# Optimization experiments

Hardware: AMD Instinct MI355X
Metric: run time of the kernel (lower is better)

Reference implementation:

```python
import jax, jax.numpy as jnp
import numpy as np

# Model dims (see shape_source): seq_len fixed to 12 by reshape(1,12,-1); rnn_units fixed to 64 by proj in-dim.
B, T, N, HZ = 16, 12, 512, 12
DIN, DOUT, YCOV = 1, 1, 1
RNN, MEMN, MEMD, K = 64, 20, 64, 3
DDEC = RNN + MEMD  # 128


def _cheb(g, k):
    # Chebyshev polynomials T_0..T_{k-1} of support g: [I, g, 2g T_{i-1} - T_{i-2}, ...]
    n = g.shape[0]
    Ts = [jnp.eye(n, dtype=g.dtype), g]
    for _ in range(2, k):
        Ts.append(2.0 * g @ Ts[-1] - Ts[-2])
    return Ts


def _agcn(x, sup, W, b):
    # x: [B,N,C], sup: [2K,N,N] -> x_g: [B,N,2K*C] (k-major order matches torch.cat over support_set)
    b_, n, _ = x.shape
    xg = jnp.einsum('knm,bmc->bnkc', sup, x).reshape(b_, n, -1)
    return xg @ W + b


def _cell(x, state, sup, gW, gb, uW, ub, hdim):
    ins = jnp.concatenate([x, state], axis=-1)
    zr = jax.nn.sigmoid(_agcn(ins, sup, gW, gb))
    z, r = zr[..., :hdim], zr[..., hdim:]
    hc = jnp.tanh(_agcn(jnp.concatenate([x, z * state], axis=-1), sup, uW, ub))
    return r * state + (1.0 - r) * hc


def setup_inputs() -> dict:
    key = jax.random.key(0)
    ks = jax.random.split(key, 16)
    def nrm(k, shape, s=0.1):
        return jax.random.normal(k, shape, dtype=jnp.float32) * s
    return {
        'x': nrm(ks[0], (B, T, N, DIN), 1.0),
        'y_cov': nrm(ks[1], (B, HZ, N, YCOV), 1.0),
        'Memory': nrm(ks[2], (MEMN, MEMD)),
        'Wq': nrm(ks[3], (RNN, MEMD)),
        'We1': nrm(ks[4], (N, MEMN)),
        'We2': nrm(ks[5], (N, MEMN)),
        'tWe1': nrm(ks[6], (MEMD, RNN)),
        'tWe2': nrm(ks[7], (MEMD, RNN)),
        'fc_d_W': nrm(ks[8], (DDEC, RNN)),
        'fc_e_W': nrm(ks[9], (RNN, RNN)),
        'enc_gate_W': nrm(ks[10], (2 * K * (DIN + RNN), 2 * RNN)),
        'enc_gate_b': jnp.zeros((2 * RNN,), jnp.float32),
        'enc_up_W': nrm(ks[11], (2 * K * (DIN + RNN), RNN)),
        'enc_up_b': jnp.zeros((RNN,), jnp.float32),
        'dec_gate_W': nrm(ks[12], (2 * K * (DOUT + YCOV + DDEC), 2 * DDEC)),
        'dec_gate_b': jnp.zeros((2 * DDEC,), jnp.float32),
        'dec_up_W': nrm(ks[13], (2 * K * (DOUT + YCOV + DDEC), DDEC)),
        'dec_up_b': jnp.zeros((DDEC,), jnp.float32),
        'proj_W': nrm(ks[14], (DDEC + RNN, DOUT)),
        'proj_b': jnp.zeros((DOUT,), jnp.float32),
    }


def reference(x, y_cov, Memory, Wq, We1, We2, tWe1, tWe2, fc_d_W, fc_e_W,
              enc_gate_W, enc_gate_b, enc_up_W, enc_up_b,
              dec_gate_W, dec_gate_b, dec_up_W, dec_up_b, proj_W, proj_b):
    # adaptive supports from memory
    ne1 = We1 @ Memory
    ne2 = We2 @ Memory
    g1 = jax.nn.softmax(jax.nn.relu(ne1 @ ne2.T), axis=-1)
    g2 = jax.nn.softmax(jax.nn.relu(ne2 @ ne1.T), axis=-1)
    sup = jnp.stack(_cheb(g1, K) + _cheb(g2, K))  # [2K,N,N]

    # encoder: GRU-style graph recurrence over time via scan
    def enc_step(state, xt):
        h = _cell(xt, state, sup, enc_gate_W, enc_gate_b, enc_up_W, enc_up_b, RNN)
        return h, h
    s0 = jnp.zeros((B, N, RNN), x.dtype)
    _, hs = jax.lax.scan(enc_step, s0, jnp.swapaxes(x, 0, 1))
    h_en = jnp.swapaxes(hs, 0, 1)  # [B,T,N,RNN]
    h_t = h_en[:, -1]

    # memory retrieval
    query = h_t @ Wq                                    # [B,N,MEMD]
    att_score = jax.nn.softmax(query @ Memory.T, axis=-1)  # [B,N,MEMN]
    h_att = att_score @ Memory                          # [B,N,MEMD]
    _, ind = jax.lax.top_k(att_score, 20)
    pos = Memory[ind[:, :, 0]]
    neg = Memory[ind[:, :, 1:]]

    # test-time supports from last-batch retrieved memory (as in torch code: h_att[-1])
    ne3 = h_att[-1] @ tWe1
    ne4 = h_att[-1] @ tWe2
    tg1 = jax.nn.softmax(jax.nn.relu(ne3 @ ne4.T), axis=-1)
    tg2 = jax.nn.softmax(jax.nn.relu(ne4 @ ne3.T), axis=-1)
    tsup = jnp.stack(_cheb(tg1, K) + _cheb(tg2, K))

    ht = jnp.concatenate([h_t, h_att], axis=-1)  # [B,N,DDEC]
    # matches torch fc_e(h_en).reshape(1,12,-1): row-major flatten of [B,T,N,RNN] into [T, B*N*RNN]
    e_flat = (h_en @ fc_e_W).reshape(T, -1)

    go = jnp.zeros((B, N, DOUT), x.dtype)
    state = ht  # num_layers = 1
    outs = []
    for t in range(HZ):
        xt = jnp.concatenate([go, y_cov[:, t]], axis=-1)
        h_de = _cell(xt, state, tsup, dec_gate_W, dec_gate_b, dec_up_W, dec_up_b, DDEC)
        state = h_de
        d_flat = (h_de @ fc_d_W).reshape(-1)            # [B*N*RNN]
        att = jax.nn.softmax(e_flat @ d_flat)           # [T] global temporal weights
        context = jnp.einsum('btnr,t->bnr', h_en, att)  # [B,N,RNN]
        go = jnp.concatenate([h_de, context], axis=-1) @ proj_W + proj_b
        outs.append(go)
    output = jnp.stack(outs, axis=1)  # [B,HZ,N,DOUT]
    return output, h_att, query, pos, neg, att_score
```

## Files before the change

kernel.cpp:

```cpp
#include <hip/hip_runtime.h>
#include <hip/hip_bf16.h>
#include <math.h>

typedef __hip_bfloat16 bf16;
typedef __attribute__((ext_vector_type(8))) short short8;
typedef __attribute__((ext_vector_type(4))) float f32x4;
typedef unsigned short u16;

__device__ inline u16 f2bu(float f) {
  unsigned u = __builtin_bit_cast(unsigned, f);
  u += 0x7fffu + ((u >> 16) & 1u);
  return (u16)(u >> 16);
}

__global__ void detect_k(const u16* __restrict__ u, int* __restrict__ flag) {
  if (threadIdx.x == 0 && blockIdx.x == 0) {
    int wild = 0;
    for (int i = 0; i < 256; i++) {
      int e = (u[i] >> 7) & 0xFF;
      if (e < 0x66 || e > 0x8A) wild++;
    }
    *flag = (wild > 64) ? 1 : 0;
  }
}

__global__ void in2f_k(const void* __restrict__ in, float* __restrict__ out, int n,
                       const int* __restrict__ flag) {
  int i = blockIdx.x * 256 + threadIdx.x;
  if (i >= n) return;
  if (*flag) out[i] = ((const float*)in)[i];
  else       out[i] = __bfloat162float(((const bf16*)in)[i]);
}

__global__ void zero_k(float* __restrict__ p, int n) {
  int i = blockIdx.x * 256 + threadIdx.x;
  if (i < n) p[i] = 0.f;
}

__global__ void zeroi_k(int* __restrict__ p, int n) {
  int i = blockIdx.x * 256 + threadIdx.x;
  if (i < n) p[i] = 0;
}

__global__ void transpose_k(const float* __restrict__ in, float* __restrict__ out,
                            int rows, int cols) {
  int i = blockIdx.x * 256 + threadIdx.x;
  if (i >= rows * cols) return;
  int c = i % cols, r = i / cols;
  out[(size_t)c * rows + r] = in[i];
}

__global__ void f2b_k(const float* __restrict__ in, u16* __restrict__ out, int n) {
  int i = blockIdx.x * 256 + threadIdx.x;
  if (i < n) out[i] = f2bu(in[i]);
}

__global__ void padw_k(const float* __restrict__ W, float* __restrict__ Wp,
                       int K, int N, int Kpad) {
  int i = blockIdx.x * 256 + threadIdx.x;
  if (i >= Kpad * N) return;
  int n = i % N, k = i / N;
  Wp[i] = (k < K) ? W[(size_t)k * N + n] : 0.f;
}

__global__ void w2bt_k(const float* __restrict__ W, u16* __restrict__ WT,
                       int KT, int Nw, int KTpad) {
  int i = blockIdx.x * 256 + threadIdx.x;
  if (i >= Nw * KTpad) return;
  int kp = i % KTpad, n = i / KTpad;
  WT[i] = (kp < KT) ? f2bu(W[(size_t)kp * Nw + n]) : (u16)0;
}

enum { EPI_NONE = 0, EPI_RELU = 1, EPI_SIG = 2, EPI_CHEB = 3, EPI_SCAT = 4, EPI_UPD = 5 };

struct GemmArgs {
  const float* A; const float* Bm; float* C;
  int M, N, K;
};
__global__ __launch_bounds__(256) void gemm_s(GemmArgs g) {
  __shared__ float As[16][65];
  __shared__ float Bs[16][65];
  const int tid = threadIdx.x;
  const int tx = tid & 15, ty = tid >> 4;
  const int bm = blockIdx.y * 64, bn = blockIdx.x * 64;
  float acc[4][4] = {{0.f}};
  for (int k0 = 0; k0 < g.K; k0 += 16) {
#pragma unroll
    for (int i = 0; i < 4; i++) {
      int idx = i * 256 + tid; int c = idx & 15, r = idx >> 4;
      int mm = bm + r, kk = k0 + c;
      As[c][r] = (mm < g.M && kk < g.K) ? g.A[(size_t)mm * g.K + kk] : 0.f;
    }
#pragma unroll
    for (int i = 0; i < 4; i++) {
      int idx = i * 256 + tid; int c = idx & 63, r = idx >> 6;
      int kk = k0 + r, nn = bn + c;
      Bs[r][c] = (kk < g.K && nn < g.N) ? g.Bm[(size_t)kk * g.N + nn] : 0.f;
    }
    __syncthreads();
#pragma unroll
    for (int kk = 0; kk < 16; kk++) {
      float a[4], b[4];
#pragma unroll
      for (int i = 0; i < 4; i++) a[i] = As[kk][ty * 4 + i];
#pragma unroll
      for (int j = 0; j < 4; j++) b[j] = Bs[kk][tx * 4 + j];
#pragma unroll
      for (int i = 0; i < 4; i++)
#pragma unroll
        for (int j = 0; j < 4; j++) acc[i][j] = fmaf(a[i], b[j], acc[i][j]);
    }
    __syncthreads();
  }
#pragma unroll
  for (int i = 0; i < 4; i++) {
    int m = bm + ty * 4 + i;
    if (m >= g.M) continue;
#pragma unroll
    for (int j = 0; j < 4; j++) {
      int n = bn + tx * 4 + j;
      if (n >= g.N) continue;
      g.C[(size_t)m * g.N + n] = acc[i][j];
    }
  }
}

struct FGemmArgs {
  const float* A; const float* Bm; const float* bias; float* C;
  int M, N, K, ldb;
  const float* aux0;
  float* aux1;
  float* aux2;
  int i0, i1, i2;
};

template<int EPI>
__global__ __launch_bounds__(256) void fgemm_k(FGemmArgs g) {
  __shared__ __align__(16) float As[2][32][68];
  __shared__ __align__(16) float Bs[2][32][68];
  const int tid = threadIdx.x;
  const int tx = tid & 15, ty = tid >> 4;
  const int bm = blockIdx.y * 64, bn = blockIdx.x * 64;
  const int ar = tid >> 2, ac = (tid & 3) * 4;
  const int br = tid >> 4, bc = (tid & 15) * 4;
  float acc[4][4] = {{0.f}};

  float4 av0 = *(const float4*)(g.A + (size_t)(bm + ar) * g.K + ac);
  float4 av1 = *(const float4*)(g.A + (size_t)(bm + ar) * g.K + 16 + ac);
  float4 bv0 = *(const float4*)(g.Bm + (size_t)br * g.ldb + bn + bc);
  float4 bv1 = *(const float4*)(g.Bm + (size_t)(16 + br) * g.ldb + bn + bc);
  As[0][ac + 0][ar] = av0.x; As[0][ac + 1][ar] = av0.y;
  As[0][ac + 2][ar] = av0.z; As[0][ac + 3][ar] = av0.w;
  As[0][16 + ac + 0][ar] = av1.x; As[0][16 + ac + 1][ar] = av1.y;
  As[0][16 + ac + 2][ar] = av1.z; As[0][16 + ac + 3][ar] = av1.w;
  *(float4*)&Bs[0][br][bc] = bv0;
  *(float4*)&Bs[0][16 + br][bc] = bv1;
  __syncthreads();

  int cur = 0;
  for (int k0 = 0; k0 < g.K; k0 += 32) {
    const bool has_next = (k0 + 32 < g.K);
    if (has_next) {
      av0 = *(const float4*)(g.A + (size_t)(bm + ar) * g.K + k0 + 32 + ac);
      av1 = *(const float4*)(g.A + (size_t)(bm + ar) * g.K + k0 + 48 + ac);
      bv0 = *(const float4*)(g.Bm + (size_t)(k0 + 32 + br) * g.ldb + bn + bc);
      bv1 = *(const float4*)(g.Bm + (size_t)(k0 + 48 + br) * g.ldb + bn + bc);
    }
#pragma unroll
    for (int kk = 0; kk < 32; kk++) {
      float4 a4 = *(const float4*)&As[cur][kk][ty * 4];
      float4 b4 = *(const float4*)&Bs[cur][kk][tx * 4];
      float a[4] = {a4.x, a4.y, a4.z, a4.w};
      float b[4] = {b4.x, b4.y, b4.z, b4.w};
#pragma unroll
      for (int i = 0; i < 4; i++)
#pragma unroll
        for (int j = 0; j < 4; j++) acc[i][j] = fmaf(a[i], b[j], acc[i][j]);
    }
    if (has_next) {
      int nxt = cur ^ 1;
      As[nxt][ac + 0][ar] = av0.x; As[nxt][ac + 1][ar] = av0.y;
      As[nxt][ac + 2][ar] = av0.z; As[nxt][ac + 3][ar] = av0.w;
      As[nxt][16 + ac + 0][ar] = av1.x; As[nxt][16 + ac + 1][ar] = av1.y;
      As[nxt][16 + ac + 2][ar] = av1.z; As[nxt][16 + ac + 3][ar] = av1.w;
      *(float4*)&Bs[nxt][br][bc] = bv0;
      *(float4*)&Bs[nxt][16 + br][bc] = bv1;
      __syncthreads();
      cur = nxt;
    }
  }
#pragma unroll
  for (int i = 0; i < 4; i++) {
    int m = bm + ty * 4 + i;
#pragma unroll
    for (int j = 0; j < 4; j++) {
      int n = bn + tx * 4 + j;
      if (n >= g.N) continue;
      float v = acc[i][j];
      if (EPI == EPI_NONE) {
        g.C[(size_t)m * g.N + n] = v;
      } else if (EPI == EPI_RELU) {
        g.C[(size_t)m * g.N + n] = fmaxf(v, 0.f);
      } else if (EPI == EPI_SIG) {
        v += g.bias[n];
        g.C[(size_t)m * g.N + n] = 1.f / (1.f + expf(-v));
      } else if (EPI == EPI_CHEB) {
        g.C[(size_t)m * g.N + n] = 2.f * v - (m == n ? 1.f : 0.f);
      } else if (EPI == EPI_SCAT) {
        int bb = n / g.i0, cc = n % g.i0;
        int km = m >> 9;
        int kmap = km + 1 + (km >= 2 ? 1 : 0);
        int node = m & 511;
        g.aux1[((size_t)bb * 512 + node) * g.i1 + (size_t)kmap * g.i0 + cc] = v;
      } else if (EPI == EPI_UPD) {
        v = tanhf(v + g.bias[n]);
        float r = g.aux0[(size_t)m * g.i0 + g.i1 + n];
        float h = r * g.aux1[(size_t)m * g.i1 + n] + (1.f - r) * v;
        g.aux1[(size_t)m * g.i1 + n] = h;
        if (g.aux2)
          g.aux2[(((size_t)(m >> 9) * 12 + g.i2) * 512 + (m & 511)) * 64 + n] = h;
      }
    }
  }
}

template<int EPI>
__global__ __launch_bounds__(256) void fgemm32_k(FGemmArgs g) {
  __shared__ __align__(16) float As[2][16][40];
  __shared__ __align__(16) float Bs[2][16][68];
  const int tid = threadIdx.x;
  const int tx = tid & 15, ty = tid >> 4;
  const int bm = blockIdx.y * 32, bn = blockIdx.x * 64;
  const int ar = tid >> 2, ac = (tid & 3) * 4;
  const int br = tid >> 4, bc = (tid & 15) * 4;
  float acc[2][4] = {{0.f}};

  float4 av, bv;
  if (ar < 32) av = *(const float4*)(g.A + (size_t)(bm + ar) * g.K + ac);
  bv = *(const float4*)(g.Bm + (size_t)br * g.ldb + bn + bc);
  if (ar < 32) {
    As[0][ac + 0][ar] = av.x; As[0][ac + 1][ar] = av.y;
    As[0][ac + 2][ar] = av.z; As[0][ac + 3][ar] = av.w;
  }
  *(float4*)&Bs[0][br][bc] = bv;
  __syncthreads();

  int cur = 0;
  for (int k0 = 0; k0 < g.K; k0 += 16) {
    const bool has_next = (k0 + 16 < g.K);
    if (has_next) {
      if (ar < 32) av = *(const float4*)(g.A + (size_t)(bm + ar) * g.K + k0 + 16 + ac);
      bv = *(const float4*)(g.Bm + (size_t)(k0 + 16 + br) * g.ldb + bn + bc);
    }
#pragma unroll
    for (int kk = 0; kk < 16; kk++) {
      float a0 = As[cur][kk][ty * 2 + 0];
      float a1 = As[cur][kk][ty * 2 + 1];
      float4 b4 = *(const float4*)&Bs[cur][kk][tx * 4];
      float b[4] = {b4.x, b4.y, b4.z, b4.w};
#pragma unroll
      for (int j = 0; j < 4; j++) {
        acc[0][j] = fmaf(a0, b[j], acc[0][j]);
        acc[1][j] = fmaf(a1, b[j], acc[1][j]);
      }
    }
    if (has_next) {
      int nxt = cur ^ 1;
      if (ar < 32) {
        As[nxt][ac + 0][ar] = av.x; As[nxt][ac + 1][ar] = av.y;
        As[nxt][ac + 2][ar] = av.z; As[nxt][ac + 3][ar] = av.w;
      }
      *(float4*)&Bs[nxt][br][bc] = bv;
      __syncthreads();
      cur = nxt;
    }
  }
#pragma unroll
  for (int i = 0; i < 2; i++) {
    int m = bm + ty * 2 + i;
#pragma unroll
    for (int j = 0; j < 4; j++) {
      int n = bn + tx * 4 + j;
      if (n >= g.N) continue;
      float v = acc[i][j];
      if (EPI == EPI_NONE) {
        g.C[(size_t)m * g.N + n] = v;
      } else if (EPI == EPI_UPD) {
        v = tanhf(v + g.bias[n]);
        float r = g.aux0[(size_t)m * g.i0 + g.i1 + n];
        float h = r * g.aux1[(size_t)m * g.i1 + n] + (1.f - r) * v;
        g.aux1[(size_t)m * g.i1 + n] = h;
        if (g.aux2)
          g.aux2[(((size_t)(m >> 9) * 12 + g.i2) * 512 + (m & 511)) * 64 + n] = h;
      }
    }
  }
}

struct MmArgs {
  const u16* A; const u16* BT; int M, N, K;
  const float* bias; float* C;
  u16* xg;
  const float* zr; float* state; float* hen;
  int i0, i1, i2;
};

template<int EPI>
__global__ __launch_bounds__(256) void mm_k(MmArgs g) {
  __shared__ __align__(16) u16 Als[2][64][40];
  __shared__ __align__(16) u16 Bls[2][64][40];
  const int tid = threadIdx.x;
  const int w = tid >> 6, lane = tid & 63;
  const int l15 = lane & 15, lk = lane >> 4;
  const int m0 = blockIdx.y * 64, n0 = blockIdx.x * 64;
  const int srow = tid >> 2, schunk = tid & 3;
  f32x4 acc[4];
#pragma unroll
  for (int j = 0; j < 4; j++) acc[j] = (f32x4){0.f, 0.f, 0.f, 0.f};

  short8 a8 = *(const short8*)(g.A + (size_t)(m0 + srow) * g.K + schunk * 8);
  short8 b8 = (short8){0,0,0,0,0,0,0,0};
  if (n0 + srow < g.N)
    b8 = *(const short8*)(g.BT + (size_t)(n0 + srow) * g.K + schunk * 8);
  *(short8*)&Als[0][srow][schunk * 8] = a8;
  *(short8*)&Bls[0][srow][schunk * 8] = b8;
  __syncthreads();

  int cur = 0;
  for (int k0 = 0; k0 < g.K; k0 += 32) {
    const bool has_next = (k0 + 32 < g.K);
    if (has_next) {
      a8 = *(const short8*)(g.A + (size_t)(m0 + srow) * g.K + k0 + 32 + schunk * 8);
      b8 = (short8){0,0,0,0,0,0,0,0};
      if (n0 + srow < g.N)
        b8 = *(const short8*)(g.BT + (size_t)(n0 + srow) * g.K + k0 + 32 + schunk * 8);
    }
    short8 af = *(const short8*)&Als[cur][w * 16 + l15][lk * 8];
#pragma unroll
    for (int j = 0; j < 4; j++) {
      short8 bf = *(const short8*)&Bls[cur][j * 16 + l15][lk * 8];
      acc[j] = __builtin_amdgcn_mfma_f32_16x16x32_bf16(af, bf, acc[j], 0, 0, 0);
    }
    if (has_next) {
      int nxt = cur ^ 1;
      *(short8*)&Als[nxt][srow][schunk * 8] = a8;
      *(short8*)&Bls[nxt][srow][schunk * 8] = b8;
      __syncthreads();
      cur = nxt;
    }
  }

#pragma unroll
  for (int j = 0; j < 4; j++) {
    int col = n0 + j * 16 + l15;
    if (col >= g.N) continue;
#pragma unroll
    for (int r = 0; r < 4; r++) {
      int row = m0 + w * 16 + lk * 4 + r;
      float v = acc[j][r];
      if (EPI == EPI_SCAT) {
        int bb = col / g.i0, cc = col % g.i0;
        int km = row >> 9;
        int kmap = km + 1 + (km >= 2 ? 1 : 0);
        int node = row & 511;
        g.xg[((size_t)bb * 512 + node) * g.i1 + (size_t)kmap * g.i0 + cc] = f2bu(v);
      } else if (EPI == EPI_SIG) {
        v += g.bias[col];
        g.C[(size_t)row * g.N + col] = 1.f / (1.f + expf(-v));
      } else if (EPI == EPI_UPD) {
        v = tanhf(v + g.bias[col]);
        float rr = g.zr[(size_t)row * g.i0 + g.i1 + col];
        float h = rr * g.state[(size_t)row * g.i1 + col] + (1.f - rr) * v;
        g.state[(size_t)row * g.i1 + col] = h;
        if (g.hen)
          g.hen[(((size_t)(row >> 9) * 12 + g.i2) * 512 + (row & 511)) * 64 + col] = h;
      }
    }
  }
}


__global__ void buildx_k(const float* __restrict__ x1, int x1bs,
                         const float* __restrict__ state,
                         const float* __restrict__ zr,
                         float* __restrict__ X, float* __restrict__ XG,
                         int C, int hdim, int zrld) {
  int idx = blockIdx.x * 256 + threadIdx.x;
  if (idx >= 16 * 512 * C) return;
  int c = idx % C; int bn = idx / C; int n = bn & 511; int b = bn >> 9;
  float v;
  if (c == 0) v = x1[(size_t)b * x1bs + n];
  else {
    v = state[(size_t)bn * hdim + (c - 1)];
    if (zr) v *= zr[(size_t)bn * zrld + (c - 1)];
  }
  X[(size_t)n * 1088 + b * C + c] = v;
  XG[(size_t)bn * 416 + c] = v;
  XG[(size_t)bn * 416 + 3 * C + c] = v;
}

__global__ void buildx2_k(const float* __restrict__ x1, int x1bs,
                          const float* __restrict__ x2, int x2bs,
                          const float* __restrict__ state,
                          const float* __restrict__ zr,
                          u16* __restrict__ XT, u16* __restrict__ XGb,
                          int C, int NX, int hdim, int zrld, int KTpad) {
  int idx = blockIdx.x * 256 + threadIdx.x;
  if (idx >= 16 * 512 * C) return;
  int c = idx % C; int bn = idx / C; int n = bn & 511; int b = bn >> 9;
  float v;
  if (c == 0) v = x1[(size_t)b * x1bs + n];
  else if (c < NX) v = x2[(size_t)b * x2bs + n];
  else {
    v = state[(size_t)bn * hdim + (c - NX)];
    if (zr) v *= zr[(size_t)bn * zrld + (c - NX)];
  }
  u16 bv = f2bu(v);
  XT[((size_t)(b * C + c)) * 512 + n] = bv;
  XGb[(size_t)bn * KTpad + c] = bv;
  XGb[(size_t)bn * KTpad + 3 * C + c] = bv;
}

__global__ __launch_bounds__(256) void softmax512_k(const float* __restrict__ Min,
                                                    float* __restrict__ out, int colMajor) {
  int row = blockIdx.x;
  __shared__ float buf[512];
  __shared__ float red[256];
  int tid = threadIdx.x;
  for (int i = tid; i < 512; i += 256)
    buf[i] = colMajor ? Min[(size_t)i * 512 + row] : Min[(size_t)row * 512 + i];
  __syncthreads();
  float mx = -1e30f;
  for (int i = tid; i < 512; i += 256) mx = fmaxf(mx, buf[i]);
  red[tid] = mx; __syncthreads();
  for (int w = 128; w > 0; w >>= 1) { if (tid < w) red[tid] = fmaxf(red[tid], red[tid + w]); __syncthreads(); }
  mx = red[0]; __syncthreads();
  float s = 0.f;
  for (int i = tid; i < 512; i += 256) { float e = expf(buf[i] - mx); buf[i] = e; s += e; }
  red[tid] = s; __syncthreads();
  for (int w = 128; w > 0; w >>= 1) { if (tid < w) red[tid] += red[tid + w]; __syncthreads(); }
  float inv = 1.f / red[0];
  for (int i = tid; i < 512; i += 256) out[(size_t)row * 512 + i] = buf[i] * inv;
}

__global__ __launch_bounds__(256) void attmem_k(const float* __restrict__ query,
    const float* __restrict__ Mem, float* __restrict__ att_out,
    float* __restrict__ hatt, int* __restrict__ ind) {
  __shared__ float sm[20 * 64];
  for (int i = threadIdx.x; i < 20 * 64; i += 256) sm[i] = Mem[i];
  __syncthreads();
  int bn = blockIdx.x * 256 + threadIdx.x;
  if (bn >= 16 * 512) return;
  float q[64];
#pragma unroll
  for (int d = 0; d < 64; d++) q[d] = query[(size_t)bn * 64 + d];
  float lg[20];
  float mx = -1e30f;
#pragma unroll
  for (int m = 0; m < 20; m++) {
    float s = 0.f;
#pragma unroll
    for (int d = 0; d < 64; d++) s = fmaf(q[d], sm[m * 64 + d], s);
    lg[m] = s; mx = fmaxf(mx, s);
  }
  float se = 0.f;
#pragma unroll
  for (int m = 0; m < 20; m++) { lg[m] = expf(lg[m] - mx); se += lg[m]; }
  float inv = 1.f / se;
#pragma unroll
  for (int m = 0; m < 20; m++) {
    lg[m] *= inv;
    att_out[(size_t)bn * 20 + m] = lg[m];
  }
#pragma unroll
  for (int d = 0; d < 64; d++) {
    float s = 0.f;
#pragma unroll
    for (int m = 0; m < 20; m++) s = fmaf(lg[m], sm[m * 64 + d], s);
    hatt[(size_t)bn * 64 + d] = s;
  }
  unsigned used = 0;
  for (int s = 0; s < 20; s++) {
    float bv = -1e30f; int bi = 0;
#pragma unroll
    for (int m = 0; m < 20; m++) {
      bool better = (!((used >> m) & 1u)) && (lg[m] > bv);
      if (better) { bv = lg[m]; bi = m; }
    }
    used |= (1u << bi);
    ind[(size_t)bn * 20 + s] = bi;
  }
}

__global__ void gather_pn_k(const int* __restrict__ ind, const float* __restrict__ Memf,
                            float* __restrict__ pos, float* __restrict__ neg) {
  size_t i = (size_t)blockIdx.x * 256 + threadIdx.x;
  if (i >= (size_t)16 * 512 * 20 * 64) return;
  int d = (int)(i & 63); size_t r = i >> 6;
  int s = (int)(r % 20); size_t bn = r / 20;
  int m = ind[bn * 20 + s];
  float v = Memf[m * 64 + d];
  if (s == 0) pos[bn * 64 + d] = v;
  else neg[(bn * 19 + (size_t)(s - 1)) * 64 + d] = v;
}

__global__ void sinit_k(const float* __restrict__ H, const float* __restrict__ hatt,
                        float* __restrict__ S) {
  int i = blockIdx.x * 256 + threadIdx.x;
  if (i >= 8192 * 128) return;
  int c = i & 127; int bn = i >> 7;
  S[i] = (c < 64) ? H[(size_t)bn * 64 + c] : hatt[(size_t)bn * 64 + (c - 64)];
}

__global__ __launch_bounds__(256) void att_dot_k(const float* __restrict__ E,
    const float* __restrict__ D, float* __restrict__ partial) {
  int t = blockIdx.y, ch = blockIdx.x;
  const float* e = E + (size_t)t * 524288 + (size_t)ch * 16384;
  const float* d = D + (size_t)ch * 16384;
  float s = 0.f;
  for (int i = threadIdx.x; i < 16384; i += 256) s = fmaf(e[i], d[i], s);
  __shared__ float red[256];
  red[threadIdx.x] = s; __syncthreads();
  for (int w = 128; w > 0; w >>= 1) {
    if (threadIdx.x < w) red[threadIdx.x] += red[threadIdx.x + w];
    __syncthreads();
  }
  if (threadIdx.x == 0) partial[t * 32 + ch] = red[0];
}

__global__ void att_sm_k(const float* __restrict__ partial, float* __restrict__ att) {
  __shared__ float p[384];
  __shared__ float l[12];
  int tid = threadIdx.x;
  p[tid] = partial[tid];
  __syncthreads();
  if (tid < 12) {
    float s = 0.f;
    for (int i = 0; i < 32; i++) s += p[tid * 32 + i];
    l[tid] = s;
  }
  __syncthreads();
  if (tid == 0) {
    float mx = l[0];
    for (int i = 1; i < 12; i++) mx = fmaxf(mx, l[i]);
    float se = 0.f; float e[12];
    for (int i = 0; i < 12; i++) { e[i] = expf(l[i] - mx); se += e[i]; }
    float inv = 1.f / se;
    for (int i = 0; i < 12; i++) att[i] = e[i] * inv;
  }
}

__global__ __launch_bounds__(64) void ctxgo_k(const float* __restrict__ hen,
    const float* __restrict__ att, const float* __restrict__ S,
    const float* __restrict__ pW, const float* __restrict__ pb,
    float* __restrict__ go, float* __restrict__ outp, int tstep) {
  int bn = blockIdx.x; int r = threadIdx.x;
  __shared__ float a[12];
  if (r < 12) a[r] = att[r];
  __syncthreads();
  int b = bn >> 9, n = bn & 511;
  float ctx = 0.f;
#pragma unroll
  for (int t = 0; t < 12; t++)
    ctx = fmaf(hen[((size_t)(b * 12 + t) * 512 + n) * 64 + r], a[t], ctx);
  float part = ctx * pW[128 + r] + S[(size_t)bn * 128 + r] * pW[r]
             + S[(size_t)bn * 128 + 64 + r] * pW[64 + r];
#pragma unroll
  for (int off = 32; off > 0; off >>= 1) part += __shfl_down(part, off);
  if (r == 0) {
    float gv = part + pb[0];
    go[bn] = gv;
    outp[(size_t)(b * 12 + tstep) * 512 + n] = gv;
  }
}


static void fgemm(hipStream_t st, int epi, const float* A, const float* Bm,
                  const float* bias, float* C, int M, int N, int K, int ldb,
                  const float* aux0, float* aux1, float* aux2,
                  int i0, int i1, int i2) {
  FGemmArgs a{A, Bm, bias, C, M, N, K, ldb, aux0, aux1, aux2, i0, i1, i2};
  dim3 grid((N + 63) / 64, M / 64);
  switch (epi) {
    case 0: fgemm_k<0><<<grid, 256, 0, st>>>(a); break;
    case 1: fgemm_k<1><<<grid, 256, 0, st>>>(a); break;
    case 2: fgemm_k<2><<<grid, 256, 0, st>>>(a); break;
    case 3: fgemm_k<3><<<grid, 256, 0, st>>>(a); break;
    case 4: fgemm_k<4><<<grid, 256, 0, st>>>(a); break;
    case 5: fgemm_k<5><<<grid, 256, 0, st>>>(a); break;
  }
}

static void fgemm32(hipStream_t st, int epi, const float* A, const float* Bm,
                    const float* bias, float* C, int M, int N, int K, int ldb,
                    const float* aux0, float* aux1, float* aux2,
                    int i0, int i1, int i2) {
  FGemmArgs a{A, Bm, bias, C, M, N, K, ldb, aux0, aux1, aux2, i0, i1, i2};
  dim3 grid((N + 63) / 64, M / 32);
  switch (epi) {
    case 0: fgemm32_k<0><<<grid, 256, 0, st>>>(a); break;
    case 5: fgemm32_k<5><<<grid, 256, 0, st>>>(a); break;
  }
}

static void mm(hipStream_t st, int epi, const u16* A, const u16* BT,
               int M, int N, int K, const float* bias, float* C, u16* xg,
               const float* zr, float* state, float* hen, int i0, int i1, int i2) {
  MmArgs a{A, BT, M, N, K, bias, C, xg, zr, state, hen, i0, i1, i2};
  dim3 grid((N + 63) / 64, M / 64);
  switch (epi) {
    case EPI_SIG:  mm_k<EPI_SIG><<<grid, 256, 0, st>>>(a); break;
    case EPI_SCAT: mm_k<EPI_SCAT><<<grid, 256, 0, st>>>(a); break;
    case EPI_UPD:  mm_k<EPI_UPD><<<grid, 256, 0, st>>>(a); break;
  }
}

extern "C" void kernel_launch(void* const* d_in, const int* in_sizes, int n_in,
                              void* d_out, int out_size, void* d_ws, size_t ws_size,
                              hipStream_t stream) {
  (void)out_size; (void)ws_size; (void)n_in; (void)in_sizes;
  float* ws = (float*)d_ws;
  float* out = (float*)d_out;

  size_t off = 0;
  auto alloc = [&](size_t n) { size_t o = off; off += (n + 63) & ~(size_t)63; return ws + o; };

  const int isz[20] = {98304, 98304, 1280, 4096, 10240, 10240, 4096, 4096, 8192, 4096,
                       49920, 128, 24960, 64, 199680, 256, 99840, 128, 192, 1};
  float* fin[20];
  for (int i = 0; i < 20; i++) fin[i] = alloc((size_t)isz[i]);

  float* Gbig  = alloc((size_t)2048 * 512);
  float* tGbig = Gbig;
  float* Mbuf  = alloc((size_t)512 * 512);
  float* ne1b  = alloc((size_t)512 * 64);
  float* ne2b  = alloc((size_t)512 * 64);
  float* neT   = alloc((size_t)64 * 512);
  float* X     = alloc((size_t)512 * 1088);
  float* XG    = alloc((size_t)8192 * 416);
  float* Wgp   = alloc((size_t)416 * 128);
  float* Wup   = alloc((size_t)416 * 64);
  float* zr    = alloc((size_t)8192 * 256);
  float* H     = alloc((size_t)8192 * 64);
  float* S     = alloc((size_t)8192 * 128);
  float* hen   = alloc((size_t)16 * 12 * 512 * 64);
  float* E     = alloc((size_t)16 * 12 * 512 * 64);
  float* Dflat = alloc((size_t)8192 * 64);
  float* go    = alloc((size_t)8192);
  float* partial = alloc((size_t)512);
  float* attv  = alloc((size_t)64);
  int* ind     = (int*)alloc((size_t)8192 * 20);
  int* dflag   = (int*)alloc((size_t)64);
  u16* Gb16 = (u16*)alloc((size_t)2048 * 512 / 2);
  u16* XT   = (u16*)alloc((size_t)2080 * 512 / 2);
  u16* XGb  = (u16*)alloc((size_t)8192 * 800 / 2);
  u16* WTdg = (u16*)alloc((size_t)256 * 800 / 2);
  u16* WTdu = (u16*)alloc((size_t)128 * 800 / 2);

  float* o_out   = out;
  float* o_hatt  = out + 98304;
  float* o_query = o_hatt + 524288;
  float* o_pos   = o_query + 524288;
  float* o_neg   = o_pos + 524288;
  float* o_att   = o_neg + 9961472;

  detect_k<<<1, 64, 0, stream>>>((const u16*)d_in[0], dflag);
  for (int i = 0; i < 20; i++)
    in2f_k<<<(isz[i] + 255) / 256, 256, 0, stream>>>(d_in[i], fin[i], isz[i], dflag);

  padw_k<<<(416 * 128 + 255) / 256, 256, 0, stream>>>(fin[10], Wgp, 390, 128, 416);
  padw_k<<<(416 * 64 + 255) / 256, 256, 0, stream>>>(fin[12], Wup, 390, 64, 416);
  w2bt_k<<<(256 * 800 + 255) / 256, 256, 0, stream>>>(fin[14], WTdg, 780, 256, 800);
  w2bt_k<<<(128 * 800 + 255) / 256, 256, 0, stream>>>(fin[16], WTdu, 780, 128, 800);

  zero_k<<<(512 * 1088 + 255) / 256, 256, 0, stream>>>(X, 512 * 1088);
  zero_k<<<(8192 * 416 + 255) / 256, 256, 0, stream>>>(XG, 8192 * 416);

  {
    GemmArgs a1{fin[4], fin[2], ne1b, 512, 64, 20};
    gemm_s<<<dim3(1, 8), 256, 0, stream>>>(a1);
    GemmArgs a2{fin[5], fin[2], ne2b, 512, 64, 20};
    gemm_s<<<dim3(1, 8), 256, 0, stream>>>(a2);
  }
  transpose_k<<<(512 * 64 + 255) / 256, 256, 0, stream>>>(ne2b, neT, 512, 64);
  fgemm(stream, EPI_RELU, ne1b, neT, nullptr, Mbuf, 512, 512, 64, 512,
        nullptr, nullptr, nullptr, 0, 0, 0);
  softmax512_k<<<512, 256, 0, stream>>>(Mbuf, Gbig, 0);
  softmax512_k<<<512, 256, 0, stream>>>(Mbuf, Gbig + (size_t)1024 * 512, 1);
  fgemm(stream, EPI_CHEB, Gbig, Gbig, nullptr, Gbig + (size_t)512 * 512,
        512, 512, 512, 512, nullptr, nullptr, nullptr, 0, 0, 0);
  fgemm(stream, EPI_CHEB, Gbig + (size_t)1024 * 512, Gbig + (size_t)1024 * 512, nullptr,
        Gbig + (size_t)1536 * 512, 512, 512, 512, 512, nullptr, nullptr, nullptr, 0, 0, 0);

  zero_k<<<(8192 * 64 + 255) / 256, 256, 0, stream>>>(H, 8192 * 64);
  zero_k<<<(8192 + 255) / 256, 256, 0, stream>>>(go, 8192);

  for (int t = 0; t < 12; t++) {
    buildx_k<<<(16 * 512 * 65 + 255) / 256, 256, 0, stream>>>(
        fin[0] + t * 512, 6144, H, nullptr, X, XG, 65, 64, 128);
    fgemm(stream, EPI_SCAT, Gbig, X, nullptr, nullptr, 2048, 1040, 512, 1088,
          nullptr, XG, nullptr, 65, 416, 0);
    fgemm(stream, EPI_SIG, XG, Wgp, fin[11], zr, 8192, 128, 416, 128,
          nullptr, nullptr, nullptr, 0, 0, 0);
    buildx_k<<<(16 * 512 * 65 + 255) / 256, 256, 0, stream>>>(
        fin[0] + t * 512, 6144, H, zr, X, XG, 65, 64, 128);
    fgemm(stream, EPI_SCAT, Gbig, X, nullptr, nullptr, 2048, 1040, 512, 1088,
          nullptr, XG, nullptr, 65, 416, 0);
    fgemm32(stream, EPI_UPD, XG, Wup, fin[13], nullptr, 8192, 64, 416, 64,
            zr, H, hen, 128, 64, t);
  }

  fgemm(stream, EPI_NONE, H, fin[3], nullptr, o_query, 8192, 64, 64, 64,
        nullptr, nullptr, nullptr, 0, 0, 0);
  attmem_k<<<32, 256, 0, stream>>>(o_query, fin[2], o_att, o_hatt, ind);
  gather_pn_k<<<(16 * 512 * 20 * 64 + 255) / 256, 256, 0, stream>>>(
      ind, fin[2], o_pos, o_neg);

  fgemm(stream, EPI_NONE, hen, fin[9], nullptr, E, 98304, 64, 64, 64,
        nullptr, nullptr, nullptr, 0, 0, 0);

  fgemm(stream, EPI_NONE, o_hatt + (size_t)15 * 512 * 64, fin[6], nullptr, ne1b,
        512, 64, 64, 64, nullptr, nullptr, nullptr, 0, 0, 0);
  fgemm(stream, EPI_NONE, o_hatt + (size_t)15 * 512 * 64, fin[7], nullptr, ne2b,
        512, 64, 64, 64, nullptr, nullptr, nullptr, 0, 0, 0);
  transpose_k<<<(512 * 64 + 255) / 256, 256, 0, stream>>>(ne2b, neT, 512, 64);
  fgemm(stream, EPI_RELU, ne1b, neT, nullptr, Mbuf, 512, 512, 64, 512,
        nullptr, nullptr, nullptr, 0, 0, 0);
  softmax512_k<<<512, 256, 0, stream>>>(Mbuf, tGbig, 0);
  softmax512_k<<<512, 256, 0, stream>>>(Mbuf, tGbig + (size_t)1024 * 512, 1);
  fgemm(stream, EPI_CHEB, tGbig, tGbig, nullptr, tGbig + (size_t)512 * 512,
        512, 512, 512, 512, nullptr, nullptr, nullptr, 0, 0, 0);
  fgemm(stream, EPI_CHEB, tGbig + (size_t)1024 * 512, tGbig + (size_t)1024 * 512, nullptr,
        tGbig + (size_t)1536 * 512, 512, 512, 512, 512, nullptr, nullptr, nullptr, 0, 0, 0);
  f2b_k<<<(2048 * 512 + 255) / 256, 256, 0, stream>>>(tGbig, Gb16, 2048 * 512);

  sinit_k<<<(8192 * 128 + 255) / 256, 256, 0, stream>>>(H, o_hatt, S);
  zeroi_k<<<(8192 * 800 / 2 + 255) / 256, 256, 0, stream>>>((int*)XGb, 8192 * 800 / 2);

  for (int t = 0; t < 12; t++) {
    buildx2_k<<<(16 * 512 * 130 + 255) / 256, 256, 0, stream>>>(
        go, 512, fin[1] + t * 512, 6144, S, nullptr, XT, XGb, 130, 2, 128, 0, 800);
    mm(stream, EPI_SCAT, Gb16, XT, 2048, 2080, 512, nullptr, nullptr, XGb,
       nullptr, nullptr, nullptr, 130, 800, 0);
    mm(stream, EPI_SIG, XGb, WTdg, 8192, 256, 800, fin[15], zr, nullptr,
       nullptr, nullptr, nullptr, 0, 0, 0);
    buildx2_k<<<(16 * 512 * 130 + 255) / 256, 256, 0, stream>>>(
        go, 512, fin[1] + t * 512, 6144, S, zr, XT, XGb, 130, 2, 128, 256, 800);
    mm(stream, EPI_SCAT, Gb16, XT, 2048, 2080, 512, nullptr, nullptr, XGb,
       nullptr, nullptr, nullptr, 130, 800, 0);
    mm(stream, EPI_UPD, XGb, WTdu, 8192, 128, 800, fin[17], nullptr, nullptr,
       zr, S, nullptr, 256, 128, 0);
    fgemm32(stream, EPI_NONE, S, fin[8], nullptr, Dflat, 8192, 64, 128, 64,
            nullptr, nullptr, nullptr, 0, 0, 0);
    att_dot_k<<<dim3(32, 12), 256, 0, stream>>>(E, Dflat, partial);
    att_sm_k<<<1, 384, 0, stream>>>(partial, attv);
    ctxgo_k<<<8192, 64, 0, stream>>>(hen, attv, S, fin[18], fin[19], go, o_out, t);
  }
}
```

Measured before the change: 3.546 ms.

## Fuse GRU input assembly into GEMM epilogues and drop buildx kernels

Removes the buildx/buildx2 kernels that rebuilt the concatenated [x, state] and [x, z*state] inputs each step. The sigmoid and update GEMM epilogues now write z*state and the new hidden state straight into the transposed and graph-expanded input buffers. Small per-step kernels fill only the exogenous input columns. The encoder gate GEMM moves to the 32-row tile variant so it can use this epilogue. This saves launches and a full read/write pass per step, at the cost of scattered, uncoalesced stores in the epilogues.

After: 3.417 ms. 3.7% less time.

```diff
diff --git a/kernel.cpp b/kernel.cpp
--- a/kernel.cpp
+++ b/kernel.cpp
@@ -131,6 +131,8 @@
   const float* aux0;
   float* aux1;
   float* aux2;
+  float* aux3;
+  float* aux4;
   int i0, i1, i2;
 };
 
@@ -201,9 +203,6 @@
         g.C[(size_t)m * g.N + n] = v;
       } else if (EPI == EPI_RELU) {
         g.C[(size_t)m * g.N + n] = fmaxf(v, 0.f);
-      } else if (EPI == EPI_SIG) {
-        v += g.bias[n];
-        g.C[(size_t)m * g.N + n] = 1.f / (1.f + expf(-v));
       } else if (EPI == EPI_CHEB) {
         g.C[(size_t)m * g.N + n] = 2.f * v - (m == n ? 1.f : 0.f);
       } else if (EPI == EPI_SCAT) {
@@ -212,13 +211,6 @@
         int kmap = km + 1 + (km >= 2 ? 1 : 0);
         int node = m & 511;
         g.aux1[((size_t)bb * 512 + node) * g.i1 + (size_t)kmap * g.i0 + cc] = v;
-      } else if (EPI == EPI_UPD) {
-        v = tanhf(v + g.bias[n]);
-        float r = g.aux0[(size_t)m * g.i0 + g.i1 + n];
-        float h = r * g.aux1[(size_t)m * g.i1 + n] + (1.f - r) * v;
-        g.aux1[(size_t)m * g.i1 + n] = h;
-        if (g.aux2)
-          g.aux2[(((size_t)(m >> 9) * 12 + g.i2) * 512 + (m & 511)) * 64 + n] = h;
       }
     }
   }
@@ -278,6 +270,7 @@
 #pragma unroll
   for (int i = 0; i < 2; i++) {
     int m = bm + ty * 2 + i;
+    int node = m & 511, bb = m >> 9;
 #pragma unroll
     for (int j = 0; j < 4; j++) {
       int n = bn + tx * 4 + j;
@@ -285,13 +278,26 @@
       float v = acc[i][j];
       if (EPI == EPI_NONE) {
         g.C[(size_t)m * g.N + n] = v;
+      } else if (EPI == EPI_SIG) {
+        v += g.bias[n];
+        float sg = 1.f / (1.f + expf(-v));
+        g.C[(size_t)m * g.N + n] = sg;
+        if (n < 64) {
+          float zh = sg * g.aux0[(size_t)m * 64 + n];
+          g.aux3[(size_t)node * 1088 + bb * 65 + 1 + n] = zh;
+          g.aux4[(size_t)m * 416 + 1 + n] = zh;
+          g.aux4[(size_t)m * 416 + 196 + n] = zh;
+        }
       } else if (EPI == EPI_UPD) {
         v = tanhf(v + g.bias[n]);
         float r = g.aux0[(size_t)m * g.i0 + g.i1 + n];
         float h = r * g.aux1[(size_t)m * g.i1 + n] + (1.f - r) * v;
         g.aux1[(size_t)m * g.i1 + n] = h;
         if (g.aux2)
-          g.aux2[(((size_t)(m >> 9) * 12 + g.i2) * 512 + (m & 511)) * 64 + n] = h;
+          g.aux2[(((size_t)bb * 12 + g.i2) * 512 + node) * 64 + n] = h;
+        g.aux3[(size_t)node * 1088 + bb * 65 + 1 + n] = h;
+        g.aux4[(size_t)m * 416 + 1 + n] = h;
+        g.aux4[(size_t)m * 416 + 196 + n] = h;
       }
     }
   }
@@ -302,6 +308,7 @@
   const float* bias; float* C;
   u16* xg;
   const float* zr; float* state; float* hen;
+  u16* xtw; u16* xgw;
   int i0, i1, i2;
 };
 
@@ -357,68 +364,59 @@
 #pragma unroll
     for (int r = 0; r < 4; r++) {
       int row = m0 + w * 16 + lk * 4 + r;
+      int node = row & 511, bb = row >> 9;
       float v = acc[j][r];
       if (EPI == EPI_SCAT) {
-        int bb = col / g.i0, cc = col % g.i0;
+        int b2 = col / g.i0, cc = col % g.i0;
         int km = row >> 9;
         int kmap = km + 1 + (km >= 2 ? 1 : 0);
-        int node = row & 511;
-        g.xg[((size_t)bb * 512 + node) * g.i1 + (size_t)kmap * g.i0 + cc] = f2bu(v);
+        g.xg[((size_t)b2 * 512 + node) * g.i1 + (size_t)kmap * g.i0 + cc] = f2bu(v);
       } else if (EPI == EPI_SIG) {
         v += g.bias[col];
-        g.C[(size_t)row * g.N + col] = 1.f / (1.f + expf(-v));
+        float sg = 1.f / (1.f + expf(-v));
+        g.C[(size_t)row * g.N + col] = sg;
+        if (col < 128) {
+          float zh = sg * g.state[(size_t)row * 128 + col];
+          u16 bv = f2bu(zh);
+          g.xtw[((size_t)(bb * 130 + 2 + col)) * 512 + node] = bv;
+          g.xgw[(size_t)row * 800 + 2 + col] = bv;
+          g.xgw[(size_t)row * 800 + 392 + col] = bv;
+        }
       } else if (EPI == EPI_UPD) {
         v = tanhf(v + g.bias[col]);
         float rr = g.zr[(size_t)row * g.i0 + g.i1 + col];
         float h = rr * g.state[(size_t)row * g.i1 + col] + (1.f - rr) * v;
         g.state[(size_t)row * g.i1 + col] = h;
-        if (g.hen)
-          g.hen[(((size_t)(row >> 9) * 12 + g.i2) * 512 + (row & 511)) * 64 + col] = h;
+        u16 bv = f2bu(h);
+        g.xtw[((size_t)(bb * 130 + 2 + col)) * 512 + node] = bv;
+        g.xgw[(size_t)row * 800 + 2 + col] = bv;
+        g.xgw[(size_t)row * 800 + 392 + col] = bv;
       }
     }
   }
 }
 
 
-__global__ void buildx_k(const float* __restrict__ x1, int x1bs,
-                         const float* __restrict__ state,
-                         const float* __restrict__ zr,
-                         float* __restrict__ X, float* __restrict__ XG,
-                         int C, int hdim, int zrld) {
-  int idx = blockIdx.x * 256 + threadIdx.x;
-  if (idx >= 16 * 512 * C) return;
-  int c = idx % C; int bn = idx / C; int n = bn & 511; int b = bn >> 9;
-  float v;
-  if (c == 0) v = x1[(size_t)b * x1bs + n];
-  else {
-    v = state[(size_t)bn * hdim + (c - 1)];
-    if (zr) v *= zr[(size_t)bn * zrld + (c - 1)];
-  }
-  X[(size_t)n * 1088 + b * C + c] = v;
-  XG[(size_t)bn * 416 + c] = v;
-  XG[(size_t)bn * 416 + 3 * C + c] = v;
-}
-
-__global__ void buildx2_k(const float* __restrict__ x1, int x1bs,
-                          const float* __restrict__ x2, int x2bs,
-                          const float* __restrict__ state,
-                          const float* __restrict__ zr,
-                          u16* __restrict__ XT, u16* __restrict__ XGb,
-                          int C, int NX, int hdim, int zrld, int KTpad) {
-  int idx = blockIdx.x * 256 + threadIdx.x;
-  if (idx >= 16 * 512 * C) return;
-  int c = idx % C; int bn = idx / C; int n = bn & 511; int b = bn >> 9;
-  float v;
-  if (c == 0) v = x1[(size_t)b * x1bs + n];
-  else if (c < NX) v = x2[(size_t)b * x2bs + n];
-  else {
-    v = state[(size_t)bn * hdim + (c - NX)];
-    if (zr) v *= zr[(size_t)bn * zrld + (c - NX)];
-  }
-  u16 bv = f2bu(v);
-  XT[((size_t)(b * C + c)) * 512 + n] = bv;
-  XGb[(size_t)bn * KTpad + c] = bv;
-  XGb[(size_t)bn * KTpad + 3 * C + c] = bv;
+__global__ void putxe_k(const float* __restrict__ x1, float* __restrict__ X,
+                        float* __restrict__ XG) {
+  int bn = blockIdx.x * 256 + threadIdx.x;
+  if (bn >= 8192) return;
+  int n = bn & 511, b = bn >> 9;
+  float v = x1[(size_t)b * 6144 + n];
+  X[(size_t)n * 1088 + b * 65] = v;
+  XG[(size_t)bn * 416 + 0] = v;
+  XG[(size_t)bn * 416 + 195] = v;
+}
+
+__global__ void putxd_k(const float* __restrict__ yc, u16* __restrict__ XT,
+                        u16* __restrict__ XGb) {
+  int bn = blockIdx.x * 256 + threadIdx.x;
+  if (bn >= 8192) return;
+  int n = bn & 511, b = bn >> 9;
+  u16 bv = f2bu(yc[(size_t)b * 6144 + n]);
+  XT[((size_t)(b * 130 + 1)) * 512 + n] = bv;
+  XGb[(size_t)bn * 800 + 1] = bv;
+  XGb[(size_t)bn * 800 + 391] = bv;
 }
 
 __global__ __launch_bounds__(256) void softmax512_k(const float* __restrict__ Min,
@@ -505,11 +503,21 @@
 }
 
 __global__ void sinit_k(const float* __restrict__ H, const float* __restrict__ hatt,
-                        float* __restrict__ S) {
+                        float* __restrict__ S, u16* __restrict__ XT,
+                        u16* __restrict__ XGb) {
   int i = blockIdx.x * 256 + threadIdx.x;
   if (i >= 8192 * 128) return;
   int c = i & 127; int bn = i >> 7;
-  S[i] = (c < 64) ? H[(size_t)bn * 64 + c] : hatt[(size_t)bn * 64 + (c - 64)];
+  int n = bn & 511, b = bn >> 9;
+  float v = (c < 64) ? H[(size_t)bn * 64 + c] : hatt[(size_t)bn * 64 + (c - 64)];
+  S[i] = v;
+  u16 bv = f2bu(v);
+  XT[((size_t)(b * 130 + 2 + c)) * 512 + n] = bv;
+  XGb[(size_t)bn * 800 + 2 + c] = bv;
+  XGb[(size_t)bn * 800 + 392 + c] = bv;
+  if (c == 0) {
+    XT[((size_t)(b * 130)) * 512 + n] = 0;
+  }
 }
 
 __global__ __launch_bounds__(256) void att_dot_k(const float* __restrict__ E,
@@ -553,7 +561,8 @@
 __global__ __launch_bounds__(64) void ctxgo_k(const float* __restrict__ hen,
     const float* __restrict__ att, const float* __restrict__ S,
     const float* __restrict__ pW, const float* __restrict__ pb,
-    float* __restrict__ go, float* __restrict__ outp, int tstep) {
+    u16* __restrict__ XT, u16* __restrict__ XGb,
+    float* __restrict__ outp, int tstep) {
   int bn = blockIdx.x; int r = threadIdx.x;
   __shared__ float a[12];
   if (r < 12) a[r] = att[r];
@@ -569,44 +578,47 @@
   for (int off = 32; off > 0; off >>= 1) part += __shfl_down(part, off);
   if (r == 0) {
     float gv = part + pb[0];
-    go[bn] = gv;
     outp[(size_t)(b * 12 + tstep) * 512 + n] = gv;
+    u16 bv = f2bu(gv);
+    XT[((size_t)(b * 130)) * 512 + n] = bv;
+    XGb[(size_t)bn * 800 + 0] = bv;
+    XGb[(size_t)bn * 800 + 390] = bv;
   }
 }
 
 
 static void fgemm(hipStream_t st, int epi, const float* A, const float* Bm,
                   const float* bias, float* C, int M, int N, int K, int ldb,
-                  const float* aux0, float* aux1, float* aux2,
+                  const float* aux0, float* aux1, float* aux2, float* aux3, float* aux4,
                   int i0, int i1, int i2) {
-  FGemmArgs a{A, Bm, bias, C, M, N, K, ldb, aux0, aux1, aux2, i0, i1, i2};
+  FGemmArgs a{A, Bm, bias, C, M, N, K, ldb, aux0, aux1, aux2, aux3, aux4, i0, i1, i2};
   dim3 grid((N + 63) / 64, M / 64);
   switch (epi) {
     case 0: fgemm_k<0><<<grid, 256, 0, st>>>(a); break;
     case 1: fgemm_k<1><<<grid, 256, 0, st>>>(a); break;
-    case 2: fgemm_k<2><<<grid, 256, 0, st>>>(a); break;
     case 3: fgemm_k<3><<<grid, 256, 0, st>>>(a); break;
     case 4: fgemm_k<4><<<grid, 256, 0, st>>>(a); break;
-    case 5: fgemm_k<5><<<grid, 256, 0, st>>>(a); break;
   }
 }
 
 static void fgemm32(hipStream_t st, int epi, const float* A, const float* Bm,
                     const float* bias, float* C, int M, int N, int K, int ldb,
-                    const float* aux0, float* aux1, float* aux2,
+                    const float* aux0, float* aux1, float* aux2, float* aux3, float* aux4,
                     int i0, int i1, int i2) {
-  FGemmArgs a{A, Bm, bias, C, M, N, K, ldb, aux0, aux1, aux2, i0, i1, i2};
+  FGemmArgs a{A, Bm, bias, C, M, N, K, ldb, aux0, aux1, aux2, aux3, aux4, i0, i1, i2};
   dim3 grid((N + 63) / 64, M / 32);
   switch (epi) {
     case 0: fgemm32_k<0><<<grid, 256, 0, st>>>(a); break;
+    case 2: fgemm32_k<2><<<grid, 256, 0, st>>>(a); break;
     case 5: fgemm32_k<5><<<grid, 256, 0, st>>>(a); break;
   }
 }
 
 static void mm(hipStream_t st, int epi, const u16* A, const u16* BT,
                int M, int N, int K, const float* bias, float* C, u16* xg,
-               const float* zr, float* state, float* hen, int i0, int i1, int i2) {
-  MmArgs a{A, BT, M, N, K, bias, C, xg, zr, state, hen, i0, i1, i2};
+               const float* zr, float* state, float* hen, u16* xtw, u16* xgw,
+               int i0, int i1, int i2) {
+  MmArgs a{A, BT, M, N, K, bias, C, xg, zr, state, hen, xtw, xgw, i0, i1, i2};
   dim3 grid((N + 63) / 64, M / 64);
   switch (epi) {
     case EPI_SIG:  mm_k<EPI_SIG><<<grid, 256, 0, st>>>(a); break;
@@ -646,7 +658,6 @@
   float* hen   = alloc((size_t)16 * 12 * 512 * 64);
   float* E     = alloc((size_t)16 * 12 * 512 * 64);
   float* Dflat = alloc((size_t)8192 * 64);
-  float* go    = alloc((size_t)8192);
   float* partial = alloc((size_t)512);
   float* attv  = alloc((size_t)64);
   int* ind     = (int*)alloc((size_t)8192 * 20);
@@ -684,76 +695,72 @@
   }
   transpose_k<<<(512 * 64 + 255) / 256, 256, 0, stream>>>(ne2b, neT, 512, 64);
   fgemm(stream, EPI_RELU, ne1b, neT, nullptr, Mbuf, 512, 512, 64, 512,
-        nullptr, nullptr, nullptr, 0, 0, 0);
+        nullptr, nullptr, nullptr, nullptr, nullptr, 0, 0, 0);
   softmax512_k<<<512, 256, 0, stream>>>(Mbuf, Gbig, 0);
   softmax512_k<<<512, 256, 0, stream>>>(Mbuf, Gbig + (size_t)1024 * 512, 1);
   fgemm(stream, EPI_CHEB, Gbig, Gbig, nullptr, Gbig + (size_t)512 * 512,
-        512, 512, 512, 512, nullptr, nullptr, nullptr, 0, 0, 0);
+        512, 512, 512, 512, nullptr, nullptr, nullptr, nullptr, nullptr, 0, 0, 0);
   fgemm(stream, EPI_CHEB, Gbig + (size_t)1024 * 512, Gbig + (size_t)1024 * 512, nullptr,
-        Gbig + (size_t)1536 * 512, 512, 512, 512, 512, nullptr, nullptr, nullptr, 0, 0, 0);
+        Gbig + (size_t)1536 * 512, 512, 512, 512, 512,
+        nullptr, nullptr, nullptr, nullptr, nullptr, 0, 0, 0);
 
   zero_k<<<(8192 * 64 + 255) / 256, 256, 0, stream>>>(H, 8192 * 64);
-  zero_k<<<(8192 + 255) / 256, 256, 0, stream>>>(go, 8192);
 
   for (int t = 0; t < 12; t++) {
-    buildx_k<<<(16 * 512 * 65 + 255) / 256, 256, 0, stream>>>(
-        fin[0] + t * 512, 6144, H, nullptr, X, XG, 65, 64, 128);
+    putxe_k<<<32, 256, 0, stream>>>(fin[0] + t * 512, X, XG);
     fgemm(stream, EPI_SCAT, Gbig, X, nullptr, nullptr, 2048, 1040, 512, 1088,
-          nullptr, XG, nullptr, 65, 416, 0);
-    fgemm(stream, EPI_SIG, XG, Wgp, fin[11], zr, 8192, 128, 416, 128,
-          nullptr, nullptr, nullptr, 0, 0, 0);
-    buildx_k<<<(16 * 512 * 65 + 255) / 256, 256, 0, stream>>>(
-        fin[0] + t * 512, 6144, H, zr, X, XG, 65, 64, 128);
+          nullptr, XG, nullptr, nullptr, nullptr, 65, 416, 0);
+    fgemm32(stream, EPI_SIG, XG, Wgp, fin[11], zr, 8192, 128, 416, 128,
+            H, nullptr, nullptr, X, XG, 0, 0, 0);
     fgemm(stream, EPI_SCAT, Gbig, X, nullptr, nullptr, 2048, 1040, 512, 1088,
-          nullptr, XG, nullptr, 65, 416, 0);
+          nullptr, XG, nullptr, nullptr, nullptr, 65, 416, 0);
     fgemm32(stream, EPI_UPD, XG, Wup, fin[13], nullptr, 8192, 64, 416, 64,
-            zr, H, hen, 128, 64, t);
+            zr, H, hen, X, XG, 128, 64, t);
   }
 
   fgemm(stream, EPI_NONE, H, fin[3], nullptr, o_query, 8192, 64, 64, 64,
-        nullptr, nullptr, nullptr, 0, 0, 0);
+        nullptr, nullptr, nullptr, nullptr, nullptr, 0, 0, 0);
   attmem_k<<<32, 256, 0, stream>>>(o_query, fin[2], o_att, o_hatt, ind);
   gather_pn_k<<<(16 * 512 * 20 * 64 + 255) / 256, 256, 0, stream>>>(
       ind, fin[2], o_pos, o_neg);
 
   fgemm(stream, EPI_NONE, hen, fin[9], nullptr, E, 98304, 64, 64, 64,
-        nullptr, nullptr, nullptr, 0, 0, 0);
+        nullptr, nullptr, nullptr, nullptr, nullptr, 0, 0, 0);
 
   fgemm(stream, EPI_NONE, o_hatt + (size_t)15 * 512 * 64, fin[6], nullptr, ne1b,
-        512, 64, 64, 64, nullptr, nullptr, nullptr, 0, 0, 0);
+        512, 64, 64, 64, nullptr, nullptr, nullptr, nullptr, nullptr, 0, 0, 0);
   fgemm(stream, EPI_NONE, o_hatt + (size_t)15 * 512 * 64, fin[7], nullptr, ne2b,
-        512, 64, 64, 64, nullptr, nullptr, nullptr, 0, 0, 0);
+        512, 64, 64, 64, nullptr, nullptr, nullptr, nullptr, nullptr, 0, 0, 0);
   transpose_k<<<(512 * 64 + 255) / 256, 256, 0, stream>>>(ne2b, neT, 512, 64);
   fgemm(stream, EPI_RELU, ne1b, neT, nullptr, Mbuf, 512, 512, 64, 512,
-        nullptr, nullptr, nullptr, 0, 0, 0);
+        nullptr, nullptr, nullptr, nullptr, nullptr, 0, 0, 0);
   softmax512_k<<<512, 256, 0, stream>>>(Mbuf, tGbig, 0);
   softmax512_k<<<512, 256, 0, stream>>>(Mbuf, tGbig + (size_t)1024 * 512, 1);
   fgemm(stream, EPI_CHEB, tGbig, tGbig, nullptr, tGbig + (size_t)512 * 512,
-        512, 512, 512, 512, nullptr, nullptr, nullptr, 0, 0, 0);
+        512, 512, 512, 512, nullptr, nullptr, nullptr, nullptr, nullptr, 0, 0, 0);
   fgemm(stream, EPI_CHEB, tGbig + (size_t)1024 * 512, tGbig + (size_t)1024 * 512, nullptr,
-        tGbig + (size_t)1536 * 512, 512, 512, 512, 512, nullptr, nullptr, nullptr, 0, 0, 0);
+        tGbig + (size_t)1536 * 512, 512, 512, 512, 512,
+        nullptr, nullptr, nullptr, nullptr, nullptr, 0, 0, 0);
   f2b_k<<<(2048 * 512 + 255) / 256, 256, 0, stream>>>(tGbig, Gb16, 2048 * 512);
 
-  sinit_k<<<(8192 * 128 + 255) / 256, 256, 0, stream>>>(H, o_hatt, S);
   zeroi_k<<<(8192 * 800 / 2 + 255) / 256, 256, 0, stream>>>((int*)XGb, 8192 * 800 / 2);
+  sinit_k<<<(8192 * 128 + 255) / 256, 256, 0, stream>>>(H, o_hatt, S, XT, XGb);
 
   for (int t = 0; t < 12; t++) {
-    buildx2_k<<<(16 * 512 * 130 + 255) / 256, 256, 0, stream>>>(
-        go, 512, fin[1] + t * 512, 6144, S, nullptr, XT, XGb, 130, 2, 128, 0, 800);
+    putxd_k<<<32, 256, 0, stream>>>(fin[1] + t * 512, XT, XGb);
     mm(stream, EPI_SCAT, Gb16, XT, 2048, 2080, 512, nullptr, nullptr, XGb,
-       nullptr, nullptr, nullptr, 130, 800, 0);
+       nullptr, nullptr, nullptr, nullptr, nullptr, 130, 800, 0);
     mm(stream, EPI_SIG, XGb, WTdg, 8192, 256, 800, fin[15], zr, nullptr,
-       nullptr, nullptr, nullptr, 0, 0, 0);
-    buildx2_k<<<(16 * 512 * 130 + 255) / 256, 256, 0, stream>>>(
-        go, 512, fin[1] + t * 512, 6144, S, zr, XT, XGb, 130, 2, 128, 256, 800);
+       nullptr, S, nullptr, XT, XGb, 0, 0, 0);
     mm(stream, EPI_SCAT, Gb16, XT, 2048, 2080, 512, nullptr, nullptr, XGb,
-       nullptr, nullptr, nullptr, 130, 800, 0);
+       nullptr, nullptr, nullptr, nullptr, nullptr, 130, 800, 0);
     mm(stream, EPI_UPD, XGb, WTdu, 8192, 128, 800, fin[17], nullptr, nullptr,
-       zr, S, nullptr, 256, 128, 0);
+       zr, S, nullptr, XT, XGb, 256, 128, 0);
     fgemm32(stream, EPI_NONE, S, fin[8], nullptr, Dflat, 8192, 64, 128, 64,
-            nullptr, nullptr, nullptr, 0, 0, 0);
+            nullptr, nullptr, nullptr, nullptr, nullptr, 0, 0, 0);
     att_dot_k<<<dim3(32, 12), 256, 0, stream>>>(E, Dflat, partial);
     att_sm_k<<<1, 384, 0, stream>>>(partial, attv);
-    ctxgo_k<<<8192, 64, 0, stream>>>(hen, attv, S, fin[18], fin[19], go, o_out, t);
-  }
-}
+    ctxgo_k<<<8192, 64, 0, stream>>>(hen, attv, S, fin[18], fin[19],
+                                     XT, XGb, o_out, t);
+  }
+}
```
